# Optimization experiments

Measured on AMD Instinct MI355X. Metric: run time of the kernel, lower is better.

Reference implementation:

```python
import jax, jax.numpy as jnp
import numpy as np
from jax import lax

B, CIN, COUT, H, W, K = 8, 256, 256, 64, 64, 3
KK = K * K
PAD, STRIDE = 1, 1
EPS = 1e-5


def setup_inputs() -> dict:
    key = jax.random.key(0)
    k0, k1, k2 = jax.random.split(key, 3)
    x = jax.random.normal(k0, (B, CIN, H, W), jnp.float32)
    # offset/mask predicting conv: 3*K*K output channels (o1, o2, mask)
    w_off = jax.random.normal(k1, (3 * KK, CIN, K, K), jnp.float32) * 0.01
    b_off = jnp.zeros((3 * KK,), jnp.float32)
    # main deformable conv weight
    weight = jax.random.normal(k2, (COUT, CIN, K, K), jnp.float32) / np.sqrt(CIN * KK).astype(np.float32)
    bias = jnp.zeros((COUT,), jnp.float32)
    gamma = jnp.ones((COUT,), jnp.float32)
    beta = jnp.zeros((COUT,), jnp.float32)
    return {"x": x, "w_off": w_off, "b_off": b_off, "weight": weight,
            "bias": bias, "gamma": gamma, "beta": beta}


def _bilinear_sample(img, ph, pw):
    """img: [C,H,W]; ph,pw: [KK,H,W] float sample positions. Zero outside. -> [C,KK,H,W]"""
    h0 = jnp.floor(ph).astype(jnp.int32)
    w0 = jnp.floor(pw).astype(jnp.int32)
    h1, w1 = h0 + 1, w0 + 1
    lh = ph - h0.astype(ph.dtype)
    lw = pw - w0.astype(pw.dtype)
    hh, hw = 1.0 - lh, 1.0 - lw

    def corner(hi, wi):
        valid = (hi >= 0) & (hi < H) & (wi >= 0) & (wi < W)
        hc = jnp.clip(hi, 0, H - 1)
        wc = jnp.clip(wi, 0, W - 1)
        v = img[:, hc, wc]  # [C,KK,H,W]
        return v * valid.astype(img.dtype)[None]

    return (corner(h0, w0) * (hh * hw)[None] + corner(h0, w1) * (hh * lw)[None]
            + corner(h1, w0) * (lh * hw)[None] + corner(h1, w1) * (lh * lw)[None])


def _forward(x, w_off, b_off, weight, bias, gamma, beta):
    dn = ('NCHW', 'OIHW', 'NCHW')
    # offset/mask branch (standard conv)
    om = lax.conv_general_dilated(x, w_off, (STRIDE, STRIDE), ((PAD, PAD), (PAD, PAD)),
                                  dimension_numbers=dn) + b_off[None, :, None, None]
    o1, o2, m = jnp.split(om, 3, axis=1)
    offset = jnp.concatenate([o1, o2], axis=1)          # [B, 2*KK, H, W]
    off_h = offset[:, 0::2]                             # [B, KK, H, W] dy per tap
    off_w = offset[:, 1::2]                             # [B, KK, H, W] dx per tap
    mask = jax.nn.sigmoid(m)                            # [B, KK, H, W]

    taps = jnp.arange(KK)
    base_h = (taps // K - PAD).astype(jnp.float32)[:, None, None] \
        + (jnp.arange(H, dtype=jnp.float32) * STRIDE)[None, :, None]  # [KK,H,1]
    base_w = (taps % K - PAD).astype(jnp.float32)[:, None, None] \
        + (jnp.arange(W, dtype=jnp.float32) * STRIDE)[None, None, :]  # [KK,1,W]
    ph = base_h[None] + off_h                           # [B,KK,H,W]
    pw = base_w[None] + off_w

    sampled = jax.vmap(_bilinear_sample)(x, ph, pw)     # [B,CIN,KK,H,W]
    sampled = sampled * mask[:, None]                   # modulated (DCNv2)

    y = jnp.einsum('bckhw,ock->bohw', sampled, weight.reshape(COUT, CIN, KK))
    y = y + bias[None, :, None, None]

    # BatchNorm2d (training mode: batch statistics) + ReLU
    mean = y.mean(axis=(0, 2, 3))
    var = y.var(axis=(0, 2, 3))
    yn = (y - mean[None, :, None, None]) * lax.rsqrt(var + EPS)[None, :, None, None]
    out = jax.nn.relu(gamma[None, :, None, None] * yn + beta[None, :, None, None])
    return out


def reference(x, w_off, b_off, weight, bias, gamma, beta):
    return _forward(x, w_off, b_off, weight, bias, gamma, beta)
```

## Files before the change

kernel.cpp:

```cpp
#include <hip/hip_runtime.h>
#include <cstdint>

#define BB    8
#define CIN   256
#define COUT  256
#define HH    64
#define WW    64
#define HWSZ  4096
#define NPIX  32768
#define NTAP  9

typedef __attribute__((ext_vector_type(8))) short    s16x8;
typedef __attribute__((ext_vector_type(8))) unsigned short u16x8;
typedef __attribute__((ext_vector_type(4))) unsigned short u16x4;
typedef __attribute__((ext_vector_type(4))) float    f32x4;

__device__ __forceinline__ float bf2f(unsigned short u) {
    unsigned int v = ((unsigned int)u) << 16;
    return __builtin_bit_cast(float, v);
}
__device__ __forceinline__ unsigned short f2bf(float f) {
    unsigned int u = __builtin_bit_cast(unsigned int, f);
    unsigned int r = (u + 0x7FFFu + ((u >> 16) & 1u)) >> 16;
    return (unsigned short)r;
}

__global__ void k_pack_x(const float* __restrict__ x, unsigned short* __restrict__ xT) {
    int blk = blockIdx.x;
    int b    = blk & 7;
    int rest = blk >> 3;
    int h    = rest >> 2;
    int c0   = (rest & 3) * 64;
    __shared__ float tile[64][65];
    int t = threadIdx.x;
#pragma unroll
    for (int r = 0; r < 16; ++r) {
        int idx = t + r * 256;
        int i = idx >> 6, w = idx & 63;
        tile[i][w] = x[(((b * 256 + c0 + i) * 64 + h) * 64) + w];
    }
    __syncthreads();
#pragma unroll
    for (int r = 0; r < 16; ++r) {
        int idx = t + r * 256;
        int w = idx >> 6, c = idx & 63;
        xT[((b * 64 + h) * 64 + w) * 256 + c0 + c] = f2bf(tile[c][w]);
    }
}

__global__ void k_pack_wk(const float* __restrict__ w, unsigned short* __restrict__ wT) {
    int idx = blockIdx.x * 256 + threadIdx.x;
    int j   = idx & 7;
    int q   = (idx >> 3) & 3;
    int o16 = (idx >> 5) & 15;
    int n16 = (idx >> 9) & 15;
    int kc  = (idx >> 13) & 7;
    int tp  = idx >> 16;
    int c = kc * 32 + q * 8 + j;
    int o = n16 * 16 + o16;
    wT[idx] = f2bf(w[(o * 256 + c) * 9 + tp]);
}

__global__ void k_pack_woff(const float* __restrict__ w, unsigned short* __restrict__ wT) {
    int idx = blockIdx.x * 256 + threadIdx.x;
    int c  = idx & 255;
    int j  = (idx >> 8) & 31;
    int tp = idx >> 13;
    float v = (j < 27) ? w[(j * 256 + c) * 9 + tp] : 0.f;
    wT[idx] = f2bf(v);
}

__global__ __launch_bounds__(256, 2)
void k_offconv(const unsigned short* __restrict__ xT,
               const unsigned short* __restrict__ wofT,
               const float* __restrict__ b_off,
               float* __restrict__ om) {
    int blk = blockIdx.x;
    int b = blk & 7, h = blk >> 3;
    int P0 = (b * 64 + h) * 64;
    int t = threadIdx.x;
    int lane = t & 63, wv = t >> 6;
    int p0w = wv * 16;
    int lm = lane & 15, q = lane >> 4;
    __shared__ unsigned short S3[3 * 66 * 136];

    const f32x4 FZ = {0.f, 0.f, 0.f, 0.f};
    f32x4 acc0 = FZ, acc1 = FZ;

    for (int cc = 0; cc < 2; ++cc) {
        __syncthreads();
        if (t < 96) {
            int rr = t >> 5, col = (t >> 4) & 1, c8 = (t & 15) * 8;
            u16x8 z = {0,0,0,0,0,0,0,0};
            *reinterpret_cast<u16x8*>(&S3[(rr * 66 + col * 65) * 136 + c8]) = z;
        }
#pragma unroll
        for (int r = 0; r < 12; ++r) {
            int v = t + r * 256;
            int rr = v >> 10, rem = v & 1023;
            int w = rem >> 4, c8 = (rem & 15) * 8;
            int hr = h + rr - 1;
            u16x8 d = {0,0,0,0,0,0,0,0};
            if (hr >= 0 && hr < 64)
                d = *reinterpret_cast<const u16x8*>(xT + ((b * 64 + hr) * 64 + w) * 256 + cc * 128 + c8);
            *reinterpret_cast<u16x8*>(&S3[(rr * 66 + w + 1) * 136 + c8]) = d;
        }
        __syncthreads();
#pragma unroll
        for (int tp = 0; tp < 9; ++tp) {
            int dh = tp / 3, dw = tp % 3;
            const unsigned short* wb = wofT + (tp * 32 + lm) * 256 + cc * 128;
#pragma unroll
            for (int kc = 0; kc < 4; ++kc) {
                s16x8 a = *reinterpret_cast<const s16x8*>(&S3[(dh * 66 + p0w + lm + dw) * 136 + kc * 32 + q * 8]);
                s16x8 b0 = *reinterpret_cast<const s16x8*>(wb + kc * 32 + q * 8);
                s16x8 b1 = *reinterpret_cast<const s16x8*>(wb + 16 * 256 + kc * 32 + q * 8);
                acc0 = __builtin_amdgcn_mfma_f32_16x16x32_bf16(a, b0, acc0, 0, 0, 0);
                acc1 = __builtin_amdgcn_mfma_f32_16x16x32_bf16(a, b1, acc1, 0, 0, 0);
            }
        }
    }
#pragma unroll
    for (int n = 0; n < 2; ++n) {
        int j = n * 16 + lm;
        float bj = (j < 27) ? b_off[j] : 0.f;
        f32x4 a = n ? acc1 : acc0;
#pragma unroll
        for (int i = 0; i < 4; ++i) {
            int prow = p0w + q * 4 + i;
            om[(P0 + prow) * 32 + j] = a[i] + bj;
        }
    }
}

__global__ __launch_bounds__(512, 4)
void k_main(const unsigned short* __restrict__ xT,
            const unsigned short* __restrict__ wTk,
            const float* __restrict__ om,
            const float* __restrict__ bias,
            unsigned short* __restrict__ y16,
            float* __restrict__ gsum, float* __restrict__ gssq) {
    int blk = blockIdx.x;
    int b = blk & 7, h = blk >> 3;
    int pblk = b * 64 + h;
    int P0 = pblk * 64;
    int t = threadIdx.x;
    int lane = t & 63, wv = t >> 6;
    int lm = lane & 15, q = lane >> 4;

    __shared__ unsigned short S[2][64 * 264];
    __shared__ float OMS[2048];

    {
        float4 tmp = *reinterpret_cast<const float4*>(om + P0 * 32 + t * 4);
        *reinterpret_cast<float4*>(&OMS[t * 4]) = tmp;
    }
    __syncthreads();

    if (wv >= 4) {
        int pw = wv - 4;
        int p  = pw * 16 + (lane >> 2);
        int s2 = lane & 3;
        int rb = b * 4096;
        float w00, w01, w10, w11;
        int a00, a01, a10, a11;

        auto setup = [&](int tp) {
            float oh = OMS[p * 32 + 2 * tp];
            float ow = OMS[p * 32 + 2 * tp + 1];
            float mv = OMS[p * 32 + 18 + tp];
            float mk = 1.f / (1.f + __expf(-mv));
            float ph = (float)(h + tp / 3 - 1) + oh;
            float pw_ = (float)(p + tp % 3 - 1) + ow;
            float fh0 = floorf(ph), fw0 = floorf(pw_);
            int ih0 = (int)fh0, iw0 = (int)fw0;
            float lh = ph - fh0, lw = pw_ - fw0;
            float hh = 1.f - lh, hw_ = 1.f - lw;
            bool vh0 = (ih0 >= 0) & (ih0 < 64);
            bool vh1 = (ih0 + 1 >= 0) & (ih0 + 1 < 64);
            bool vw0 = (iw0 >= 0) & (iw0 < 64);
            bool vw1 = (iw0 + 1 >= 0) & (iw0 + 1 < 64);
            w00 = hh * hw_ * mk * (float)(vh0 & vw0);
            w01 = hh * lw  * mk * (float)(vh0 & vw1);
            w10 = lh * hw_ * mk * (float)(vh1 & vw0);
            w11 = lh * lw  * mk * (float)(vh1 & vw1);
            int ch0 = min(max(ih0, 0), 63), ch1 = min(max(ih0 + 1, 0), 63);
            int cw0 = min(max(iw0, 0), 63), cw1 = min(max(iw0 + 1, 0), 63);
            a00 = ((rb + ch0 * 64 + cw0) * 256) + s2 * 8;
            a01 = ((rb + ch0 * 64 + cw1) * 256) + s2 * 8;
            a10 = ((rb + ch1 * 64 + cw0) * 256) + s2 * 8;
            a11 = ((rb + ch1 * 64 + cw1) * 256) + s2 * 8;
        };

        u16x8 rA[8], rB[8];
        auto issueQ = [&](int qq, u16x8* r) {
            int co = qq * 64;
#pragma unroll
            for (int j = 0; j < 2; ++j) {
                r[0 + j] = *reinterpret_cast<const u16x8*>(xT + a00 + co + j * 32);
                r[2 + j] = *reinterpret_cast<const u16x8*>(xT + a01 + co + j * 32);
                r[4 + j] = *reinterpret_cast<const u16x8*>(xT + a10 + co + j * 32);
                r[6 + j] = *reinterpret_cast<const u16x8*>(xT + a11 + co + j * 32);
            }
        };
        auto blendQ = [&](int buf, int qq, u16x8* r) {
#pragma unroll
            for (int j = 0; j < 2; ++j) {
                u16x8 res;
#pragma unroll
                for (int k = 0; k < 8; ++k) {
                    float v = w00 * bf2f(r[0 + j][k]);
                    v = fmaf(w01, bf2f(r[2 + j][k]), v);
                    v = fmaf(w10, bf2f(r[4 + j][k]), v);
                    v = fmaf(w11, bf2f(r[6 + j][k]), v);
                    res[k] = f2bf(v);
                }
                *reinterpret_cast<u16x8*>(&S[buf][p * 264 + qq * 64 + j * 32 + s2 * 8]) = res;
            }
        };
        auto fillTap = [&](int tp, int buf) {
            setup(tp);
            issueQ(0, rA);
            issueQ(1, rB);
            blendQ(buf, 0, rA);
            issueQ(2, rA);
            blendQ(buf, 1, rB);
            issueQ(3, rB);
            blendQ(buf, 2, rA);
            blendQ(buf, 3, rB);
        };

        fillTap(0, 0);
        __syncthreads();
        for (int tp = 0; tp < 9; ++tp) {
            if (tp < 8) fillTap(tp + 1, (tp + 1) & 1);
            __syncthreads();
        }
    } else {
        int o0 = wv * 64;
        const f32x4 FZ = {0.f, 0.f, 0.f, 0.f};
        f32x4 acc[4][4];
#pragma unroll
        for (int m = 0; m < 4; ++m)
#pragma unroll
            for (int n = 0; n < 4; ++n) acc[m][n] = FZ;

        __syncthreads();
        for (int tp = 0; tp < 9; ++tp) {
            const unsigned short* Sc = &S[tp & 1][0];
            const unsigned short* wtap = wTk + (size_t)tp * 65536
                                       + (size_t)(wv * 4) * 512 + lm * 32 + q * 8;
#pragma unroll
            for (int kc = 0; kc < 8; ++kc) {
                const unsigned short* wb = wtap + kc * 8192;
                s16x8 bf0 = *reinterpret_cast<const s16x8*>(wb);
                s16x8 bf1 = *reinterpret_cast<const s16x8*>(wb + 512);
                s16x8 bf2 = *reinterpret_cast<const s16x8*>(wb + 1024);
                s16x8 bf3 = *reinterpret_cast<const s16x8*>(wb + 1536);
#pragma unroll
                for (int mt = 0; mt < 4; ++mt) {
                    s16x8 a = *reinterpret_cast<const s16x8*>(
                        &Sc[(mt * 16 + lm) * 264 + kc * 32 + q * 8]);
                    acc[mt][0] = __builtin_amdgcn_mfma_f32_16x16x32_bf16(a, bf0, acc[mt][0], 0, 0, 0);
                    acc[mt][1] = __builtin_amdgcn_mfma_f32_16x16x32_bf16(a, bf1, acc[mt][1], 0, 0, 0);
                    acc[mt][2] = __builtin_amdgcn_mfma_f32_16x16x32_bf16(a, bf2, acc[mt][2], 0, 0, 0);
                    acc[mt][3] = __builtin_amdgcn_mfma_f32_16x16x32_bf16(a, bf3, acc[mt][3], 0, 0, 0);
                }
            }
            __syncthreads();
        }

        u16x4* yv = reinterpret_cast<u16x4*>(y16);
#pragma unroll
        for (int nt = 0; nt < 4; ++nt) {
            int o = o0 + nt * 16 + lm;
            float bo = bias[o];
            float sacc = 0.f, ssacc = 0.f;
#pragma unroll
            for (int mt = 0; mt < 4; ++mt) {
                u16x4 st;
#pragma unroll
                for (int i = 0; i < 4; ++i) {
                    float v = acc[mt][nt][i] + bo;
                    st[i] = f2bf(v);
                    sacc += v; ssacc += v * v;
                }
                int idx4 = ((pblk * 4 + wv) * 16 + nt * 4 + mt) * 64 + lane;
                yv[idx4] = st;
            }
            sacc  += __shfl_xor(sacc, 16);
            sacc  += __shfl_xor(sacc, 32);
            ssacc += __shfl_xor(ssacc, 16);
            ssacc += __shfl_xor(ssacc, 32);
            if (q == 0) {
                atomicAdd(&gsum[o], sacc);
                atomicAdd(&gssq[o], ssacc);
            }
        }
    }
}

__global__ void k_bnrelu(const unsigned short* __restrict__ y16,
                         const float* __restrict__ gsum, const float* __restrict__ gssq,
                         const float* __restrict__ gamma, const float* __restrict__ beta,
                         float* __restrict__ out) {
    int blk = blockIdx.x;
    int b = blk & 7, h = blk >> 3;
    int pblk = b * 64 + h;
    __shared__ unsigned short T[64 * 257];
    __shared__ float sc[256], sh[256];
    int t = threadIdx.x;
    {
        const float n = 32768.f;
        float mean = gsum[t] / n;
        float var = gssq[t] / n - mean * mean;
        float inv = rsqrtf(var + 1e-5f);
        float s = gamma[t] * inv;
        sc[t] = s;
        sh[t] = beta[t] - mean * s;
    }
    const u16x4* yv = reinterpret_cast<const u16x4*>(y16) + pblk * 4096;
#pragma unroll
    for (int r = 0; r < 16; ++r) {
        int v = t + r * 256;
        u16x4 d = yv[v];
        int lane = v & 63, mt = (v >> 6) & 3, nt = (v >> 8) & 3, wvv = (v >> 10) & 3;
        int p = mt * 16 + (lane >> 4) * 4;
        int o = wvv * 64 + nt * 16 + (lane & 15);
        T[(p + 0) * 257 + o] = d[0];
        T[(p + 1) * 257 + o] = d[1];
        T[(p + 2) * 257 + o] = d[2];
        T[(p + 3) * 257 + o] = d[3];
    }
    __syncthreads();
    int w = t & 63;
    int ob = (t >> 6) * 64;
    float* obase = out + (size_t)b * (256 * 4096) + h * 64 + w;
#pragma unroll 4
    for (int rr = 0; rr < 64; ++rr) {
        int o = ob + rr;
        float v = bf2f(T[w * 257 + o]);
        obase[(size_t)o * 4096] = fmaxf(v * sc[o] + sh[o], 0.f);
    }
}

extern "C" void kernel_launch(void* const* d_in, const int* in_sizes, int n_in,
                              void* d_out, int out_size, void* d_ws, size_t ws_size,
                              hipStream_t stream) {
    const float* x      = (const float*)d_in[0];
    const float* w_off  = (const float*)d_in[1];
    const float* b_off  = (const float*)d_in[2];
    const float* weight = (const float*)d_in[3];
    const float* bias   = (const float*)d_in[4];
    const float* gamma  = (const float*)d_in[5];
    const float* beta   = (const float*)d_in[6];

    char* ws = (char*)d_ws;
    const size_t OFF_XT    = 0;
    const size_t OFF_WT    = OFF_XT + 16777216;
    const size_t OFF_WOFT  = OFF_WT + 1179648;
    const size_t OFF_OM    = OFF_WOFT + 147456;
    const size_t OFF_Y16   = OFF_OM + 4194304;
    const size_t OFF_SUM   = OFF_Y16 + 16777216;
    const size_t OFF_SUMSQ = OFF_SUM + 1024;

    unsigned short* xT   = (unsigned short*)(ws + OFF_XT);
    unsigned short* wTk  = (unsigned short*)(ws + OFF_WT);
    unsigned short* wofT = (unsigned short*)(ws + OFF_WOFT);
    float* om    = (float*)(ws + OFF_OM);
    unsigned short* y16  = (unsigned short*)(ws + OFF_Y16);
    float* sum   = (float*)(ws + OFF_SUM);
    float* sumsq = (float*)(ws + OFF_SUMSQ);

    hipMemsetAsync(ws + OFF_SUM, 0, 2048, stream);

    k_pack_x   <<<2048, 256, 0, stream>>>(x, xT);
    k_pack_wk  <<<2304, 256, 0, stream>>>(weight, wTk);
    k_pack_woff<<< 288, 256, 0, stream>>>(w_off, wofT);
    k_offconv  <<< 512, 256, 0, stream>>>(xT, wofT, b_off, om);
    k_main     <<< 512, 512, 0, stream>>>(xT, wTk, om, bias, y16, sum, sumsq);
    k_bnrelu   <<< 512, 256, 0, stream>>>(y16, sum, sumsq, gamma, beta, (float*)d_out);
}
```

Before: 216.7 us.

## Vectorize packing and output stores, fuse weight packs, prefetch MFMA weights

Several unrelated changes land together. The x-pack kernel now writes 16-byte bf16 vectors, and the two weight-pack kernels are merged into one launch. In the main kernel, the offset/mask tile in shared memory is padded to 33 floats to avoid bank conflicts. The gather warps now handle two pixels each with 8 lanes per pixel, giving contiguous 128-byte channel segments. Weight fragments for the MFMA loop are double-buffered in registers, and the BN/ReLU epilogue writes float4 stores along w. These aim at memory coalescing, launch overhead and load latency, at the cost of extra registers in the gather and MFMA paths.

```diff
diff --git a/kernel.cpp b/kernel.cpp
--- a/kernel.cpp
+++ b/kernel.cpp
@@ -41,33 +41,40 @@
     }
     __syncthreads();
 #pragma unroll
-    for (int r = 0; r < 16; ++r) {
+    for (int r = 0; r < 2; ++r) {
         int idx = t + r * 256;
-        int w = idx >> 6, c = idx & 63;
-        xT[((b * 64 + h) * 64 + w) * 256 + c0 + c] = f2bf(tile[c][w]);
-    }
-}
-
-__global__ void k_pack_wk(const float* __restrict__ w, unsigned short* __restrict__ wT) {
-    int idx = blockIdx.x * 256 + threadIdx.x;
-    int j   = idx & 7;
-    int q   = (idx >> 3) & 3;
-    int o16 = (idx >> 5) & 15;
-    int n16 = (idx >> 9) & 15;
-    int kc  = (idx >> 13) & 7;
-    int tp  = idx >> 16;
-    int c = kc * 32 + q * 8 + j;
-    int o = n16 * 16 + o16;
-    wT[idx] = f2bf(w[(o * 256 + c) * 9 + tp]);
-}
-
-__global__ void k_pack_woff(const float* __restrict__ w, unsigned short* __restrict__ wT) {
-    int idx = blockIdx.x * 256 + threadIdx.x;
-    int c  = idx & 255;
-    int j  = (idx >> 8) & 31;
-    int tp = idx >> 13;
-    float v = (j < 27) ? w[(j * 256 + c) * 9 + tp] : 0.f;
-    wT[idx] = f2bf(v);
+        int w  = idx >> 3;
+        int c8 = (idx & 7) * 8;
+        u16x8 res;
+#pragma unroll
+        for (int k = 0; k < 8; ++k) res[k] = f2bf(tile[c8 + k][w]);
+        *reinterpret_cast<u16x8*>(&xT[((b * 64 + h) * 64 + w) * 256 + c0 + c8]) = res;
+    }
+}
+
+__global__ void k_pack_w2(const float* __restrict__ w, const float* __restrict__ woff,
+                          unsigned short* __restrict__ wT, unsigned short* __restrict__ wofT) {
+    int bid = blockIdx.x;
+    int t = threadIdx.x;
+    if (bid < 2304) {
+        int idx = bid * 256 + t;
+        int j   = idx & 7;
+        int q   = (idx >> 3) & 3;
+        int o16 = (idx >> 5) & 15;
+        int n16 = (idx >> 9) & 15;
+        int kc  = (idx >> 13) & 7;
+        int tp  = idx >> 16;
+        int c = kc * 32 + q * 8 + j;
+        int o = n16 * 16 + o16;
+        wT[idx] = f2bf(w[(o * 256 + c) * 9 + tp]);
+    } else {
+        int idx = (bid - 2304) * 256 + t;
+        int c  = idx & 255;
+        int j  = (idx >> 8) & 31;
+        int tp = idx >> 13;
+        float v = (j < 27) ? woff[(j * 256 + c) * 9 + tp] : 0.f;
+        wofT[idx] = f2bf(v);
+    }
 }
 
 __global__ __launch_bounds__(256, 2)
@@ -149,26 +156,33 @@
     int lm = lane & 15, q = lane >> 4;
 
     __shared__ unsigned short S[2][64 * 264];
-    __shared__ float OMS[2048];
+    __shared__ float OMS[64 * 33];
 
     {
-        float4 tmp = *reinterpret_cast<const float4*>(om + P0 * 32 + t * 4);
-        *reinterpret_cast<float4*>(&OMS[t * 4]) = tmp;
+        int v = t * 4;
+        int p = v >> 5, j = v & 31;
+        float4 tmp = *reinterpret_cast<const float4*>(om + P0 * 32 + v);
+        OMS[p * 33 + j]     = tmp.x;
+        OMS[p * 33 + j + 1] = tmp.y;
+        OMS[p * 33 + j + 2] = tmp.z;
+        OMS[p * 33 + j + 3] = tmp.w;
     }
     __syncthreads();
 
     if (wv >= 4) {
         int pw = wv - 4;
-        int p  = pw * 16 + (lane >> 2);
-        int s2 = lane & 3;
+        int s  = lane & 7;
+        int pA = pw * 16 + (lane >> 3);
+        int pB = pA + 8;
         int rb = b * 4096;
-        float w00, w01, w10, w11;
-        int a00, a01, a10, a11;
-
-        auto setup = [&](int tp) {
-            float oh = OMS[p * 32 + 2 * tp];
-            float ow = OMS[p * 32 + 2 * tp + 1];
-            float mv = OMS[p * 32 + 18 + tp];
+
+        float wgA[4], wgB[4];
+        int   adA[4], adB[4];
+
+        auto setup = [&](int tp, int p, float* wg, int* ad) {
+            float oh = OMS[p * 33 + 2 * tp];
+            float ow = OMS[p * 33 + 2 * tp + 1];
+            float mv = OMS[p * 33 + 18 + tp];
             float mk = 1.f / (1.f + __expf(-mv));
             float ph = (float)(h + tp / 3 - 1) + oh;
             float pw_ = (float)(p + tp % 3 - 1) + ow;
@@ -180,54 +194,50 @@
             bool vh1 = (ih0 + 1 >= 0) & (ih0 + 1 < 64);
             bool vw0 = (iw0 >= 0) & (iw0 < 64);
             bool vw1 = (iw0 + 1 >= 0) & (iw0 + 1 < 64);
-            w00 = hh * hw_ * mk * (float)(vh0 & vw0);
-            w01 = hh * lw  * mk * (float)(vh0 & vw1);
-            w10 = lh * hw_ * mk * (float)(vh1 & vw0);
-            w11 = lh * lw  * mk * (float)(vh1 & vw1);
+            wg[0] = hh * hw_ * mk * (float)(vh0 & vw0);
+            wg[1] = hh * lw  * mk * (float)(vh0 & vw1);
+            wg[2] = lh * hw_ * mk * (float)(vh1 & vw0);
+            wg[3] = lh * lw  * mk * (float)(vh1 & vw1);
             int ch0 = min(max(ih0, 0), 63), ch1 = min(max(ih0 + 1, 0), 63);
             int cw0 = min(max(iw0, 0), 63), cw1 = min(max(iw0 + 1, 0), 63);
-            a00 = ((rb + ch0 * 64 + cw0) * 256) + s2 * 8;
-            a01 = ((rb + ch0 * 64 + cw1) * 256) + s2 * 8;
-            a10 = ((rb + ch1 * 64 + cw0) * 256) + s2 * 8;
-            a11 = ((rb + ch1 * 64 + cw1) * 256) + s2 * 8;
+            ad[0] = ((rb + ch0 * 64 + cw0) * 256);
+            ad[1] = ((rb + ch0 * 64 + cw1) * 256);
+            ad[2] = ((rb + ch1 * 64 + cw0) * 256);
+            ad[3] = ((rb + ch1 * 64 + cw1) * 256);
         };
 
-        u16x8 rA[8], rB[8];
-        auto issueQ = [&](int qq, u16x8* r) {
-            int co = qq * 64;
-#pragma unroll
-            for (int j = 0; j < 2; ++j) {
-                r[0 + j] = *reinterpret_cast<const u16x8*>(xT + a00 + co + j * 32);
-                r[2 + j] = *reinterpret_cast<const u16x8*>(xT + a01 + co + j * 32);
-                r[4 + j] = *reinterpret_cast<const u16x8*>(xT + a10 + co + j * 32);
-                r[6 + j] = *reinterpret_cast<const u16x8*>(xT + a11 + co + j * 32);
+        u16x8 rP[4], rQ[4];
+        auto issueSet = [&](const int* ad, int j, u16x8* r) {
+            int off = j * 64 + s * 8;
+#pragma unroll
+            for (int c = 0; c < 4; ++c)
+                r[c] = *reinterpret_cast<const u16x8*>(xT + ad[c] + off);
+        };
+        auto blendSet = [&](int buf, int p, const float* wg, int j, u16x8* r) {
+            u16x8 res;
+#pragma unroll
+            for (int k = 0; k < 8; ++k) {
+                float v = wg[0] * bf2f(r[0][k]);
+                v = fmaf(wg[1], bf2f(r[1][k]), v);
+                v = fmaf(wg[2], bf2f(r[2][k]), v);
+                v = fmaf(wg[3], bf2f(r[3][k]), v);
+                res[k] = f2bf(v);
             }
-        };
-        auto blendQ = [&](int buf, int qq, u16x8* r) {
-#pragma unroll
-            for (int j = 0; j < 2; ++j) {
-                u16x8 res;
-#pragma unroll
-                for (int k = 0; k < 8; ++k) {
-                    float v = w00 * bf2f(r[0 + j][k]);
-                    v = fmaf(w01, bf2f(r[2 + j][k]), v);
-                    v = fmaf(w10, bf2f(r[4 + j][k]), v);
-                    v = fmaf(w11, bf2f(r[6 + j][k]), v);
-                    res[k] = f2bf(v);
-                }
-                *reinterpret_cast<u16x8*>(&S[buf][p * 264 + qq * 64 + j * 32 + s2 * 8]) = res;
-            }
+            *reinterpret_cast<u16x8*>(&S[buf][p * 264 + j * 64 + s * 8]) = res;
         };
         auto fillTap = [&](int tp, int buf) {
-            setup(tp);
-            issueQ(0, rA);
-            issueQ(1, rB);
-            blendQ(buf, 0, rA);
-            issueQ(2, rA);
-            blendQ(buf, 1, rB);
-            issueQ(3, rB);
-            blendQ(buf, 2, rA);
-            blendQ(buf, 3, rB);
+            setup(tp, pA, wgA, adA);
+            setup(tp, pB, wgB, adB);
+            issueSet(adA, 0, rP);
+            issueSet(adA, 1, rQ);
+            blendSet(buf, pA, wgA, 0, rP);  issueSet(adA, 2, rP);
+            blendSet(buf, pA, wgA, 1, rQ);  issueSet(adA, 3, rQ);
+            blendSet(buf, pA, wgA, 2, rP);  issueSet(adB, 0, rP);
+            blendSet(buf, pA, wgA, 3, rQ);  issueSet(adB, 1, rQ);
+            blendSet(buf, pB, wgB, 0, rP);  issueSet(adB, 2, rP);
+            blendSet(buf, pB, wgB, 1, rQ);  issueSet(adB, 3, rQ);
+            blendSet(buf, pB, wgB, 2, rP);
+            blendSet(buf, pB, wgB, 3, rQ);
         };
 
         fillTap(0, 0);
@@ -250,21 +260,26 @@
             const unsigned short* Sc = &S[tp & 1][0];
             const unsigned short* wtap = wTk + (size_t)tp * 65536
                                        + (size_t)(wv * 4) * 512 + lm * 32 + q * 8;
+            s16x8 wbuf[2][4];
+#pragma unroll
+            for (int n = 0; n < 4; ++n)
+                wbuf[0][n] = *reinterpret_cast<const s16x8*>(wtap + n * 512);
 #pragma unroll
             for (int kc = 0; kc < 8; ++kc) {
-                const unsigned short* wb = wtap + kc * 8192;
-                s16x8 bf0 = *reinterpret_cast<const s16x8*>(wb);
-                s16x8 bf1 = *reinterpret_cast<const s16x8*>(wb + 512);
-                s16x8 bf2 = *reinterpret_cast<const s16x8*>(wb + 1024);
-                s16x8 bf3 = *reinterpret_cast<const s16x8*>(wb + 1536);
+                if (kc < 7) {
+                    const unsigned short* wb = wtap + (kc + 1) * 8192;
+#pragma unroll
+                    for (int n = 0; n < 4; ++n)
+                        wbuf[(kc + 1) & 1][n] = *reinterpret_cast<const s16x8*>(wb + n * 512);
+                }
 #pragma unroll
                 for (int mt = 0; mt < 4; ++mt) {
                     s16x8 a = *reinterpret_cast<const s16x8*>(
                         &Sc[(mt * 16 + lm) * 264 + kc * 32 + q * 8]);
-                    acc[mt][0] = __builtin_amdgcn_mfma_f32_16x16x32_bf16(a, bf0, acc[mt][0], 0, 0, 0);
-                    acc[mt][1] = __builtin_amdgcn_mfma_f32_16x16x32_bf16(a, bf1, acc[mt][1], 0, 0, 0);
-                    acc[mt][2] = __builtin_amdgcn_mfma_f32_16x16x32_bf16(a, bf2, acc[mt][2], 0, 0, 0);
-                    acc[mt][3] = __builtin_amdgcn_mfma_f32_16x16x32_bf16(a, bf3, acc[mt][3], 0, 0, 0);
+#pragma unroll
+                    for (int n = 0; n < 4; ++n)
+                        acc[mt][n] = __builtin_amdgcn_mfma_f32_16x16x32_bf16(
+                            a, wbuf[kc & 1][n], acc[mt][n], 0, 0, 0);
                 }
             }
             __syncthreads();
@@ -333,14 +348,19 @@
         T[(p + 3) * 257 + o] = d[3];
     }
     __syncthreads();
-    int w = t & 63;
-    int ob = (t >> 6) * 64;
-    float* obase = out + (size_t)b * (256 * 4096) + h * 64 + w;
-#pragma unroll 4
-    for (int rr = 0; rr < 64; ++rr) {
-        int o = ob + rr;
-        float v = bf2f(T[w * 257 + o]);
-        obase[(size_t)o * 4096] = fmaxf(v * sc[o] + sh[o], 0.f);
+    int w4   = (t & 15) * 4;
+    int orow = t >> 4;
+    float* obase = out + (size_t)b * (256 * 4096) + h * 64;
+#pragma unroll
+    for (int it = 0; it < 16; ++it) {
+        int o = orow + it * 16;
+        float scl = sc[o], shf = sh[o];
+        float4 vo;
+        vo.x = fmaxf(bf2f(T[(w4 + 0) * 257 + o]) * scl + shf, 0.f);
+        vo.y = fmaxf(bf2f(T[(w4 + 1) * 257 + o]) * scl + shf, 0.f);
+        vo.z = fmaxf(bf2f(T[(w4 + 2) * 257 + o]) * scl + shf, 0.f);
+        vo.w = fmaxf(bf2f(T[(w4 + 3) * 257 + o]) * scl + shf, 0.f);
+        *reinterpret_cast<float4*>(obase + (size_t)o * 4096 + w4) = vo;
     }
 }
 
@@ -374,10 +394,9 @@
 
     hipMemsetAsync(ws + OFF_SUM, 0, 2048, stream);
 
-    k_pack_x   <<<2048, 256, 0, stream>>>(x, xT);
-    k_pack_wk  <<<2304, 256, 0, stream>>>(weight, wTk);
-    k_pack_woff<<< 288, 256, 0, stream>>>(w_off, wofT);
-    k_offconv  <<< 512, 256, 0, stream>>>(xT, wofT, b_off, om);
-    k_main     <<< 512, 512, 0, stream>>>(xT, wTk, om, bias, y16, sum, sumsq);
-    k_bnrelu   <<< 512, 256, 0, stream>>>(y16, sum, sumsq, gamma, beta, (float*)d_out);
-}
+    k_pack_x <<<2048, 256, 0, stream>>>(x, xT);
+    k_pack_w2<<<2592, 256, 0, stream>>>(weight, w_off, wTk, wofT);
+    k_offconv<<< 512, 256, 0, stream>>>(xT, wofT, b_off, om);
+    k_main   <<< 512, 512, 0, stream>>>(xT, wTk, om, bias, y16, sum, sumsq);
+    k_bnrelu <<< 512, 256, 0, stream>>>(y16, sum, sumsq, gamma, beta, (float*)d_out);
+}
```

New measurement: 211.4 us. -2.4%, faster.
